# Kernel tuning notes

Measured on AMD Instinct MI355X. Metric: run time of the kernel, lower is better.

## Reference

```python
import jax, jax.numpy as jnp
import numpy as np

DIM = 96
NUM_HEADS = 6
KSIZE = 3
DILATIONS = (1, 2, 3)
HEAD_DIM = DIM // NUM_HEADS            # 16
NUM_DIL = len(DILATIONS)
GROUP_DIM = DIM // NUM_DIL             # 32 channels per dilation branch
MLP_HIDDEN = int(DIM * 4.0)
SCALE = HEAD_DIM ** -0.5
EPS = 1e-5


def _unfold(x, k, dil):
    """nn.Unfold(k, dilation=dil, padding=dil*(k-1)//2, stride=1).
    x: (B, C, H, W) -> (B, C, k*k, H, W), kernel positions row-major."""
    B, C, H, W = x.shape
    pad = dil * (k - 1) // 2
    xp = jnp.pad(x, ((0, 0), (0, 0), (pad, pad), (pad, pad)))
    pats = [xp[:, :, i * dil:i * dil + H, j * dil:j * dil + W]
            for i in range(k) for j in range(k)]
    return jnp.stack(pats, axis=2)  # (B, C, kk, H, W)


def _layernorm(x, w, b):
    mu = jnp.mean(x, axis=-1, keepdims=True)
    var = jnp.mean(jnp.square(x - mu), axis=-1, keepdims=True)
    return (x - mu) * jax.lax.rsqrt(var + EPS) * w + b


def _dilate_attention(q, k, v, dil):
    """q,k,v: (B, GROUP_DIM, H, W) -> (B, H, W, GROUP_DIM)."""
    B, gd, H, W = q.shape
    h = gd // HEAD_DIM
    kk = KSIZE * KSIZE
    HW = H * W
    qf = q.reshape(B, h, HEAD_DIM, HW)                      # bhdn
    ku = _unfold(k, KSIZE, dil).reshape(B, h, HEAD_DIM, kk, HW)  # bhdkn
    attn = jnp.einsum('bhdn,bhdkn->bhnk', qf, ku) * SCALE   # (B,h,HW,kk)
    attn = jax.nn.softmax(attn, axis=-1)
    vu = _unfold(v, KSIZE, dil).reshape(B, h, HEAD_DIM, kk, HW)
    out = jnp.einsum('bhnk,bhdkn->bnhd', attn, vu)          # (B,HW,h,HEAD_DIM)
    return out.reshape(B, H, W, gd)


def setup_inputs() -> dict:
    key = jax.random.key(0)
    ks = jax.random.split(key, 8)
    B, H, W = 8, 128, 128
    s = 0.02
    return {
        'x': jax.random.normal(ks[0], (B, DIM, H, W), jnp.float32),
        'qkv_w': jax.random.normal(ks[1], (3 * DIM, DIM), jnp.float32) * s,
        'proj_w': jax.random.normal(ks[2], (DIM, DIM), jnp.float32) * s,
        'proj_b': jnp.zeros((DIM,), jnp.float32),
        'ln1_w': jnp.ones((DIM,), jnp.float32),
        'ln1_b': jnp.zeros((DIM,), jnp.float32),
        'ln2_w': jnp.ones((DIM,), jnp.float32),
        'ln2_b': jnp.zeros((DIM,), jnp.float32),
        'fc1_w': jax.random.normal(ks[3], (MLP_HIDDEN, DIM), jnp.float32) * s,
        'fc1_b': jnp.zeros((MLP_HIDDEN,), jnp.float32),
        'fc2_w': jax.random.normal(ks[4], (DIM, MLP_HIDDEN), jnp.float32) * s,
        'fc2_b': jnp.zeros((DIM,), jnp.float32),
    }


def reference(x, qkv_w, proj_w, proj_b, ln1_w, ln1_b, ln2_w, ln2_b,
              fc1_w, fc1_b, fc2_w, fc2_b):
    B, C, H, W = x.shape
    xhw = jnp.transpose(x, (0, 2, 3, 1))                    # (B,H,W,C)

    # --- attention branch ---
    y = _layernorm(xhw, ln1_w, ln1_b)                       # (B,H,W,C)
    # qkv 1x1 conv == per-pixel matmul; output channel layout (3, nd, gd)
    qkv = jnp.einsum('bhwc,oc->bohw', y, qkv_w)             # (B,3C,H,W)
    qkv = qkv.reshape(B, 3, NUM_DIL, GROUP_DIM, H, W)
    outs = [
        _dilate_attention(qkv[:, 0, i], qkv[:, 1, i], qkv[:, 2, i], DILATIONS[i])
        for i in range(NUM_DIL)
    ]
    attn_out = jnp.concatenate(outs, axis=-1)               # (B,H,W,C)
    attn_out = jnp.einsum('bhwc,oc->bhwo', attn_out, proj_w) + proj_b
    xhw = xhw + attn_out

    # --- MLP branch ---
    y = _layernorm(xhw, ln2_w, ln2_b)
    h1 = jax.nn.gelu(jnp.einsum('bhwc,oc->bhwo', y, fc1_w) + fc1_b,
                     approximate=False)
    mlp_out = jnp.einsum('bhwc,oc->bhwo', h1, fc2_w) + fc2_b
    xhw = xhw + mlp_out

    return jnp.transpose(xhw, (0, 3, 1, 2))                 # (B,C,H,W)
```

## Files before the change

kernel.cpp:

```cpp
#include <hip/hip_runtime.h>
#include <hip/hip_bf16.h>
#include <math.h>

typedef __attribute__((ext_vector_type(8))) short bf16x8;
typedef __attribute__((ext_vector_type(4))) float f32x4;
typedef __attribute__((ext_vector_type(2))) unsigned u32x2;

#define MTOT  131072
#define HW16K 16384

__device__ inline float bf2f(unsigned short u) {
    union { unsigned u; float f; } x; x.u = ((unsigned)u) << 16; return x.f;
}
__device__ inline unsigned short f2bf(float a) {
    __hip_bfloat16 h = __float2bfloat16(a);
    union { __hip_bfloat16 h; unsigned short u; } c; c.h = h; return c.u;
}
__device__ inline unsigned pack2bf(float a, float b) {
    __hip_bfloat162 h = __float22bfloat162_rn(make_float2(a, b));
    union { __hip_bfloat162 h; unsigned u; } c; c.h = h; return c.u;
}
__device__ inline float gelu(float v) {
    float u = v * fmaf(0.07135481f, v * v, 1.5957691f);
    return __fdividef(v, 1.f + __expf(-u));
}
__device__ inline void load16(const unsigned short* p, float* f) {
    uint4 u0 = *(const uint4*)p;
    uint4 u1 = *(const uint4*)(p + 8);
    unsigned w[8] = {u0.x, u0.y, u0.z, u0.w, u1.x, u1.y, u1.z, u1.w};
#pragma unroll
    for (int i = 0; i < 8; i++) {
        union { unsigned u; float f; } lo, hi;
        lo.u = w[i] << 16; hi.u = w[i] & 0xffff0000u;
        f[2 * i] = lo.f; f[2 * i + 1] = hi.f;
    }
}

__global__ __launch_bounds__(256) void k_prep(const float* __restrict__ qw,
                                              const float* __restrict__ pw,
                                              const float* __restrict__ f1,
                                              const float* __restrict__ f2,
                                              const float* __restrict__ pb,
                                              const float* __restrict__ l2w,
                                              const float* __restrict__ l2b,
                                              const float* __restrict__ f2b,
                                              unsigned short* __restrict__ wq,
                                              unsigned short* __restrict__ wpt,
                                              unsigned short* __restrict__ w1t,
                                              unsigned short* __restrict__ w2t,
                                              float* __restrict__ scal) {
    int t = blockIdx.x * 256 + threadIdx.x;
    if (t < 27648) {
        int row = t / 96, col = t - row * 96;
        int s = row / 96;
        int rem = row - s * 96;
        int di = rem >> 5;
        int hd = (rem >> 4) & 1;
        int c  = rem & 15;
        int nrow = s * 96 + (di * 2 + hd) * 16 + c;
        wq[nrow * 96 + col] = f2bf(qw[t]);
    }
    else if (t < 36864) {
        int t2 = t - 27648;
        int och = t2 / 96, ich = t2 - och * 96;
        int nt = ((och >> 5) << 1) + ((och >> 2) & 1);
        int j  = ((och >> 3) & 3) * 4 + (och & 3);
        wpt[((nt * 3 + (ich >> 5)) * 16 + j) * 32 + (ich & 31)] = f2bf(pw[t2]);
    }
    else if (t < 73728) {
        int t2 = t - 36864;
        int och = t2 / 96, col = t2 - och * 96;
        int f  = och >> 5;
        int p  = och & 31;
        int q  = p >> 3, tt = (p >> 2) & 1, r = p & 3;
        int tile = f * 2 + tt;
        int j = q * 4 + r;
        w1t[((tile * 3 + (col >> 5)) * 16 + j) * 32 + (col & 31)] = f2bf(f1[t2]);
    }
    else if (t < 110592) {
        int t3 = t - 73728;
        int och = t3 / 384, ich = t3 - och * 384;
        int nt = ((och >> 5) << 1) + ((och >> 2) & 1);
        int j  = ((och >> 3) & 3) * 4 + (och & 3);
        w2t[((nt * 12 + (ich >> 5)) * 16 + j) * 32 + (ich & 31)] = f2bf(f2[t3]);
    }
    else if (t < 110976) {
        int i = t - 110592;
        int s = i / 96, slot = i - s * 96;
        int nt = slot >> 4, qq = (slot >> 2) & 3, r = slot & 3;
        int c = ((nt >> 1) << 5) + qq * 8 + ((nt & 1) << 2) + r;
        const float* src = (s == 0) ? pb : (s == 1) ? l2w : (s == 2) ? l2b : f2b;
        scal[i] = src[c];
    }
}

__global__ __launch_bounds__(512) void k_ln1qkv(const float* __restrict__ x,
                                                const float* __restrict__ w,
                                                const float* __restrict__ bln,
                                                const unsigned short* __restrict__ wq,
                                                unsigned short* __restrict__ qkvb) {
    __shared__ unsigned short bufbf[256 * 100];
    __shared__ unsigned short Bs[288 * 104];
    __shared__ float ps[512], ps2[512];
    int tid = threadIdx.x;
    int gp0 = blockIdx.x * 256;
    int b = gp0 >> 14, pix0 = gp0 & 16383;
    int p = tid & 255, half = tid >> 8;

    for (int i = tid; i < 3456; i += 512) {
        int row = i / 12, col = i - row * 12;
        *(uint4*)(Bs + row * 104 + col * 8) = ((const uint4*)wq)[i];
    }

    float val[48];
    float s = 0.f, s2 = 0.f;
#pragma unroll
    for (int i = 0; i < 48; i++) {
        int c = half * 48 + i;
        float v = x[((size_t)b * 96 + c) * HW16K + pix0 + p];
        val[i] = v; s += v; s2 += v * v;
    }
    ps[tid] = s; ps2[tid] = s2;
    __syncthreads();
    float st = ps[p] + ps[p + 256];
    float st2 = ps2[p] + ps2[p + 256];
    float mu = st * (1.f / 96.f);
    float inv = rsqrtf(st2 * (1.f / 96.f) - mu * mu + 1e-5f);
#pragma unroll
    for (int i = 0; i < 24; i++) {
        int c = half * 48 + 2 * i;
        float n0 = (val[2 * i] - mu) * inv * w[c] + bln[c];
        float n1 = (val[2 * i + 1] - mu) * inv * w[c + 1] + bln[c + 1];
        *(unsigned*)(bufbf + p * 100 + c) = pack2bf(n0, n1);
    }
    __syncthreads();

    int lane = tid & 63, wv = tid >> 6;
    int q = lane >> 4, l15 = lane & 15;
#pragma unroll 1
    for (int it = 0; it < 2; it++) {
        int pxl = (wv * 2 + it) * 16 + l15;
        bf16x8 pf[3];
#pragma unroll
        for (int f = 0; f < 3; f++)
            pf[f] = *(const bf16x8*)(bufbf + pxl * 100 + q * 8 + f * 32);
        int gpx = gp0 + pxl;
#pragma unroll
        for (int nt = 0; nt < 18; nt++) {
            f32x4 acc = (f32x4){0.f, 0.f, 0.f, 0.f};
#pragma unroll
            for (int f = 0; f < 3; f++) {
                bf16x8 wf = *(const bf16x8*)(Bs + (nt * 16 + l15) * 104 + q * 8 + f * 32);
                acc = __builtin_amdgcn_mfma_f32_16x16x32_bf16(wf, pf[f], acc, 0, 0, 0);
            }
            u32x2 pk = { pack2bf(acc[0], acc[1]), pack2bf(acc[2], acc[3]) };
            __builtin_nontemporal_store(pk,
                (u32x2*)(qkvb + ((size_t)nt * MTOT + gpx) * 16 + q * 4));
        }
    }
}

__global__ __launch_bounds__(256) void k_attn(const unsigned short* __restrict__ qkvb,
                                              unsigned short* __restrict__ attnb) {
    int bid = blockIdx.x;
    int xcd = bid & 7;
    int idx = bid >> 3;
    int g   = idx >> 6;
    int yb  = (xcd << 6) | (idx & 63);
    int px  = yb * 256 + threadIdx.x;

    int d = (g >> 1) + 1;
    int pix = px & 16383;
    int hh = pix >> 7, ww = pix & 127;
    int ibase = px & ~16383;

    const unsigned short* qpl = qkvb + (size_t)g * (MTOT * 16);
    const unsigned short* kpl = qkvb + (size_t)(6 + g) * (MTOT * 16);
    const unsigned short* vpl = qkvb + (size_t)(12 + g) * (MTOT * 16);

    float q[16];
    load16(qpl + (size_t)px * 16, q);

    float sc[9]; int nloc[9]; bool ok[9];
#pragma unroll
    for (int i = 0; i < 3; i++) {
#pragma unroll
        for (int j = 0; j < 3; j++) {
            int k9 = i * 3 + j;
            int yy = hh + (i - 1) * d;
            int xx = ww + (j - 1) * d;
            bool o_ = ((unsigned)yy < 128u) && ((unsigned)xx < 128u);
            ok[k9] = o_;
            nloc[k9] = ibase + yy * 128 + xx;
            float s = 0.f;
            if (o_) {
                float kf[16];
                load16(kpl + (size_t)nloc[k9] * 16, kf);
#pragma unroll
                for (int c = 0; c < 16; c++) s += q[c] * kf[c];
            }
            sc[k9] = s * 0.25f;
        }
    }
    float mx = sc[0];
#pragma unroll
    for (int k9 = 1; k9 < 9; k9++) mx = fmaxf(mx, sc[k9]);
    float sum = 0.f;
#pragma unroll
    for (int k9 = 0; k9 < 9; k9++) { sc[k9] = __expf(sc[k9] - mx); sum += sc[k9]; }
    float rs = 1.f / sum;

    float o[16];
#pragma unroll
    for (int c = 0; c < 16; c++) o[c] = 0.f;
#pragma unroll
    for (int k9 = 0; k9 < 9; k9++) {
        if (ok[k9]) {
            float vf[16];
            load16(vpl + (size_t)nloc[k9] * 16, vf);
            float w9 = sc[k9];
#pragma unroll
            for (int c = 0; c < 16; c++) o[c] += w9 * vf[c];
        }
    }
    uint4* orow = (uint4*)(attnb + ((size_t)g * MTOT + px) * 16);
    uint4 pk0;
    pk0.x = pack2bf(o[0] * rs, o[1] * rs);
    pk0.y = pack2bf(o[2] * rs, o[3] * rs);
    pk0.z = pack2bf(o[4] * rs, o[5] * rs);
    pk0.w = pack2bf(o[6] * rs, o[7] * rs);
    orow[0] = pk0;
    uint4 pk1;
    pk1.x = pack2bf(o[8] * rs, o[9] * rs);
    pk1.y = pack2bf(o[10] * rs, o[11] * rs);
    pk1.z = pack2bf(o[12] * rs, o[13] * rs);
    pk1.w = pack2bf(o[14] * rs, o[15] * rs);
    orow[1] = pk1;
}

__global__ __launch_bounds__(256) void k_pmlp(const unsigned short* __restrict__ attnb,
                                              const unsigned short* __restrict__ wpt,
                                              const float* __restrict__ scal,
                                              const float* __restrict__ x,
                                              const unsigned short* __restrict__ w1t,
                                              const float* __restrict__ b1,
                                              const unsigned short* __restrict__ w2t,
                                              float* __restrict__ out) {
    int tid = threadIdx.x;
    int lane = tid & 63, wv = tid >> 6;
    int q = lane >> 4, l15 = lane & 15;
    int pt0 = (blockIdx.x * 4 + wv) * 2;
    int px0 = pt0 * 16 + l15;
    int px1 = px0 + 16;

    float v0[24], v1[24];
    bf16x8 a0[3], a1[3];

#define PROJ_TILE(PX, V, A)                                                      \
    do {                                                                         \
        bf16x8 pf[3];                                                            \
        _Pragma("unroll")                                                        \
        for (int f = 0; f < 3; f++) {                                            \
            int pa = 2 * f + (q >> 1);                                           \
            pf[f] = *(const bf16x8*)(attnb + ((size_t)pa * MTOT + (PX)) * 16 + (q & 1) * 8); \
        }                                                                        \
        f32x4 acc[6];                                                            \
        _Pragma("unroll")                                                        \
        for (int nt = 0; nt < 6; nt++) acc[nt] = (f32x4){0.f, 0.f, 0.f, 0.f};    \
        _Pragma("unroll")                                                        \
        for (int nt = 0; nt < 6; nt++) {                                         \
            _Pragma("unroll")                                                    \
            for (int kf = 0; kf < 3; kf++) {                                     \
                bf16x8 wf = *(const bf16x8*)(wpt + ((nt * 3 + kf) * 16 + l15) * 32 + q * 8); \
                acc[nt] = __builtin_amdgcn_mfma_f32_16x16x32_bf16(wf, pf[kf], acc[nt], 0, 0, 0); \
            }                                                                    \
        }                                                                        \
        int bb_ = (PX) >> 14, pix_ = (PX) & 16383;                               \
        float s_ = 0.f, s2_ = 0.f;                                               \
        _Pragma("unroll")                                                        \
        for (int nt = 0; nt < 6; nt++) {                                         \
            float4 pbq = ((const float4*)scal)[nt * 4 + q];                      \
            int cb = ((nt >> 1) << 5) + q * 8 + ((nt & 1) << 2);                 \
            _Pragma("unroll")                                                    \
            for (int r = 0; r < 4; r++) {                                        \
                float xv = x[((size_t)bb_ * 96 + cb + r) * HW16K + pix_];        \
                float t_ = acc[nt][r] + ((&pbq.x)[r]) + xv;                      \
                V[nt * 4 + r] = t_; s_ += t_; s2_ += t_ * t_;                    \
            }                                                                    \
        }                                                                        \
        s_ += __shfl_xor(s_, 16);  s_ += __shfl_xor(s_, 32);                     \
        s2_ += __shfl_xor(s2_, 16); s2_ += __shfl_xor(s2_, 32);                  \
        float mu_ = s_ * (1.f / 96.f);                                           \
        float inv_ = rsqrtf(s2_ * (1.f / 96.f) - mu_ * mu_ + 1e-5f);             \
        float nrm[24];                                                           \
        _Pragma("unroll")                                                        \
        for (int nt = 0; nt < 6; nt++) {                                         \
            float4 lwq = ((const float4*)(scal + 96))[nt * 4 + q];               \
            float4 lbq = ((const float4*)(scal + 192))[nt * 4 + q];              \
            _Pragma("unroll")                                                    \
            for (int r = 0; r < 4; r++)                                          \
                nrm[nt * 4 + r] = (V[nt * 4 + r] - mu_) * inv_ * ((&lwq.x)[r]) + ((&lbq.x)[r]); \
        }                                                                        \
        _Pragma("unroll")                                                        \
        for (int kf = 0; kf < 3; kf++) {                                         \
            union { unsigned u[4]; bf16x8 v; } Hh;                               \
            Hh.u[0] = pack2bf(nrm[(kf * 2) * 4 + 0], nrm[(kf * 2) * 4 + 1]);     \
            Hh.u[1] = pack2bf(nrm[(kf * 2) * 4 + 2], nrm[(kf * 2) * 4 + 3]);     \
            Hh.u[2] = pack2bf(nrm[(kf * 2 + 1) * 4 + 0], nrm[(kf * 2 + 1) * 4 + 1]); \
            Hh.u[3] = pack2bf(nrm[(kf * 2 + 1) * 4 + 2], nrm[(kf * 2 + 1) * 4 + 3]); \
            A[kf] = Hh.v;                                                        \
        }                                                                        \
    } while (0)

    PROJ_TILE(px0, v0, a0);
    PROJ_TILE(px1, v1, a1);
#undef PROJ_TILE

    f32x4 acc2a[6], acc2b[6];
#pragma unroll
    for (int nt = 0; nt < 6; nt++) {
        acc2a[nt] = (f32x4){0.f, 0.f, 0.f, 0.f};
        acc2b[nt] = (f32x4){0.f, 0.f, 0.f, 0.f};
    }

#pragma unroll 1
    for (int f = 0; f < 12; f++) {
        bf16x8 wf0[3], wf1[3];
#pragma unroll
        for (int kf = 0; kf < 3; kf++) {
            wf0[kf] = *(const bf16x8*)(w1t + (((2 * f) * 3 + kf) * 16 + l15) * 32 + q * 8);
            wf1[kf] = *(const bf16x8*)(w1t + (((2 * f + 1) * 3 + kf) * 16 + l15) * 32 + q * 8);
        }
        f32x4 c00 = (f32x4){0.f,0.f,0.f,0.f}, c01 = (f32x4){0.f,0.f,0.f,0.f};
        f32x4 c10 = (f32x4){0.f,0.f,0.f,0.f}, c11 = (f32x4){0.f,0.f,0.f,0.f};
#pragma unroll
        for (int kf = 0; kf < 3; kf++) {
            c00 = __builtin_amdgcn_mfma_f32_16x16x32_bf16(wf0[kf], a0[kf], c00, 0, 0, 0);
            c01 = __builtin_amdgcn_mfma_f32_16x16x32_bf16(wf1[kf], a0[kf], c01, 0, 0, 0);
            c10 = __builtin_amdgcn_mfma_f32_16x16x32_bf16(wf0[kf], a1[kf], c10, 0, 0, 0);
            c11 = __builtin_amdgcn_mfma_f32_16x16x32_bf16(wf1[kf], a1[kf], c11, 0, 0, 0);
        }
        bf16x8 w2f[6];
#pragma unroll
        for (int nt = 0; nt < 6; nt++)
            w2f[nt] = *(const bf16x8*)(w2t + ((nt * 12 + f) * 16 + l15) * 32 + q * 8);

        float4 bb0 = ((const float4*)b1)[8 * f + 2 * q];
        float4 bb1 = ((const float4*)b1)[8 * f + 2 * q + 1];
        union { unsigned u[4]; bf16x8 v; } H0, H1;
        H0.u[0] = pack2bf(gelu(c00[0] + bb0.x), gelu(c00[1] + bb0.y));
        H0.u[1] = pack2bf(gelu(c00[2] + bb0.z), gelu(c00[3] + bb0.w));
        H0.u[2] = pack2bf(gelu(c01[0] + bb1.x), gelu(c01[1] + bb1.y));
        H0.u[3] = pack2bf(gelu(c01[2] + bb1.z), gelu(c01[3] + bb1.w));
        H1.u[0] = pack2bf(gelu(c10[0] + bb0.x), gelu(c10[1] + bb0.y));
        H1.u[1] = pack2bf(gelu(c10[2] + bb0.z), gelu(c10[3] + bb0.w));
        H1.u[2] = pack2bf(gelu(c11[0] + bb1.x), gelu(c11[1] + bb1.y));
        H1.u[3] = pack2bf(gelu(c11[2] + bb1.z), gelu(c11[3] + bb1.w));

#pragma unroll
        for (int nt = 0; nt < 6; nt++) {
            acc2a[nt] = __builtin_amdgcn_mfma_f32_16x16x32_bf16(w2f[nt], H0.v, acc2a[nt], 0, 0, 0);
            acc2b[nt] = __builtin_amdgcn_mfma_f32_16x16x32_bf16(w2f[nt], H1.v, acc2b[nt], 0, 0, 0);
        }
    }

    int b0 = px0 >> 14, pia = px0 & 16383;
    int b1i = px1 >> 14, pib = px1 & 16383;
#pragma unroll
    for (int nt = 0; nt < 6; nt++) {
        float4 b2q = ((const float4*)(scal + 288))[nt * 4 + q];
        int cb = ((nt >> 1) << 5) + q * 8 + ((nt & 1) << 2);
#pragma unroll
        for (int r = 0; r < 4; r++) {
            float ov0 = acc2a[nt][r] + ((&b2q.x)[r]) + v0[nt * 4 + r];
            __builtin_nontemporal_store(ov0, out + ((size_t)b0 * 96 + cb + r) * HW16K + pia);
            float ov1 = acc2b[nt][r] + ((&b2q.x)[r]) + v1[nt * 4 + r];
            __builtin_nontemporal_store(ov1, out + ((size_t)b1i * 96 + cb + r) * HW16K + pib);
        }
    }
}

extern "C" void kernel_launch(void* const* d_in, const int* in_sizes, int n_in,
                              void* d_out, int out_size, void* d_ws, size_t ws_size,
                              hipStream_t stream) {
    const float* x      = (const float*)d_in[0];
    const float* qkv_w  = (const float*)d_in[1];
    const float* proj_w = (const float*)d_in[2];
    const float* proj_b = (const float*)d_in[3];
    const float* ln1w   = (const float*)d_in[4];
    const float* ln1b   = (const float*)d_in[5];
    const float* ln2w   = (const float*)d_in[6];
    const float* ln2b   = (const float*)d_in[7];
    const float* fc1w   = (const float*)d_in[8];
    const float* fc1b   = (const float*)d_in[9];
    const float* fc2w   = (const float*)d_in[10];
    const float* fc2b   = (const float*)d_in[11];
    float* out = (float*)d_out;

    char* ws = (char*)d_ws;
    unsigned short* wq   = (unsigned short*)(ws);
    unsigned short* wpt  = (unsigned short*)(ws + 55296);
    unsigned short* w1t  = (unsigned short*)(ws + 73728);
    unsigned short* w2t  = (unsigned short*)(ws + 147456);
    float*          scal = (float*)(ws + 221184);
    unsigned short* rA   = (unsigned short*)(ws + 230400);
    unsigned short* qkvb = (unsigned short*)(ws + 25396224);

    k_prep<<<434, 256, 0, stream>>>(qkv_w, proj_w, fc1w, fc2w,
                                    proj_b, ln2w, ln2b, fc2b,
                                    wq, wpt, w1t, w2t, scal);

    k_ln1qkv<<<512, 512, 0, stream>>>(x, ln1w, ln1b, wq, qkvb);
    k_attn<<<3072, 256, 0, stream>>>(qkvb, rA);
    k_pmlp<<<1024, 256, 0, stream>>>(rA, wpt, scal, x, w1t, fc1b, w2t, out);
}
```

Baseline: 238.8 us.

## Pre-tile QKV weights, enlarge LN1-QKV blocks, and use shuffle-based LayerNorm reduction

QKV weights are now written by the prep kernel in MFMA-tile order, so they can be copied to LDS contiguously without padding. The LN1+QKV kernel now uses 1024-thread blocks covering 512 pixels, with each wave owning 32 pixels split into two channel halves. The mean/variance reduction uses a cross-lane shuffle instead of shared memory plus a barrier. This lowers how many times the weights are staged per pixel and removes a sync, but the LDS footprint grows to about 154KB, limiting occupancy to one block per CU.

Measured after the change: 286.5 us. +20.0%, slower.

```diff
diff --git a/kernel.cpp b/kernel.cpp
--- a/kernel.cpp
+++ b/kernel.cpp
@@ -44,7 +44,7 @@
                                               const float* __restrict__ l2w,
                                               const float* __restrict__ l2b,
                                               const float* __restrict__ f2b,
-                                              unsigned short* __restrict__ wq,
+                                              unsigned short* __restrict__ wqt,
                                               unsigned short* __restrict__ wpt,
                                               unsigned short* __restrict__ w1t,
                                               unsigned short* __restrict__ w2t,
@@ -58,7 +58,8 @@
         int hd = (rem >> 4) & 1;
         int c  = rem & 15;
         int nrow = s * 96 + (di * 2 + hd) * 16 + c;
-        wq[nrow * 96 + col] = f2bf(qw[t]);
+        wqt[(((nrow >> 4) * 3 + (col >> 5)) * 16 + (nrow & 15)) * 32 + (col & 31)]
+            = f2bf(qw[t]);
     }
     else if (t < 36864) {
         int t2 = t - 27648;
@@ -94,23 +95,22 @@
     }
 }
 
-__global__ __launch_bounds__(512) void k_ln1qkv(const float* __restrict__ x,
-                                                const float* __restrict__ w,
-                                                const float* __restrict__ bln,
-                                                const unsigned short* __restrict__ wq,
-                                                unsigned short* __restrict__ qkvb) {
-    __shared__ unsigned short bufbf[256 * 100];
-    __shared__ unsigned short Bs[288 * 104];
-    __shared__ float ps[512], ps2[512];
+__global__ __launch_bounds__(1024) void k_ln1qkv(const float* __restrict__ x,
+                                                 const float* __restrict__ w,
+                                                 const float* __restrict__ bln,
+                                                 const unsigned short* __restrict__ wqt,
+                                                 unsigned short* __restrict__ qkvb) {
+    __shared__ unsigned short bufbf[512 * 100];
+    __shared__ unsigned short Bs[288 * 96];
     int tid = threadIdx.x;
-    int gp0 = blockIdx.x * 256;
+    int gp0 = blockIdx.x * 512;
     int b = gp0 >> 14, pix0 = gp0 & 16383;
-    int p = tid & 255, half = tid >> 8;
-
-    for (int i = tid; i < 3456; i += 512) {
-        int row = i / 12, col = i - row * 12;
-        *(uint4*)(Bs + row * 104 + col * 8) = ((const uint4*)wq)[i];
-    }
+    int lane = tid & 63, wv = tid >> 6;
+    int half = lane >> 5;
+    int p = wv * 32 + (lane & 31);
+
+    for (int i = tid; i < 3456; i += 1024)
+        ((uint4*)Bs)[i] = ((const uint4*)wqt)[i];
 
     float val[48];
     float s = 0.f, s2 = 0.f;
@@ -120,12 +120,10 @@
         float v = x[((size_t)b * 96 + c) * HW16K + pix0 + p];
         val[i] = v; s += v; s2 += v * v;
     }
-    ps[tid] = s; ps2[tid] = s2;
-    __syncthreads();
-    float st = ps[p] + ps[p + 256];
-    float st2 = ps2[p] + ps2[p + 256];
-    float mu = st * (1.f / 96.f);
-    float inv = rsqrtf(st2 * (1.f / 96.f) - mu * mu + 1e-5f);
+    s += __shfl_xor(s, 32);
+    s2 += __shfl_xor(s2, 32);
+    float mu = s * (1.f / 96.f);
+    float inv = rsqrtf(s2 * (1.f / 96.f) - mu * mu + 1e-5f);
 #pragma unroll
     for (int i = 0; i < 24; i++) {
         int c = half * 48 + 2 * i;
@@ -135,7 +133,6 @@
     }
     __syncthreads();
 
-    int lane = tid & 63, wv = tid >> 6;
     int q = lane >> 4, l15 = lane & 15;
 #pragma unroll 1
     for (int it = 0; it < 2; it++) {
@@ -149,9 +146,9 @@
         for (int nt = 0; nt < 18; nt++) {
             f32x4 acc = (f32x4){0.f, 0.f, 0.f, 0.f};
 #pragma unroll
-            for (int f = 0; f < 3; f++) {
-                bf16x8 wf = *(const bf16x8*)(Bs + (nt * 16 + l15) * 104 + q * 8 + f * 32);
-                acc = __builtin_amdgcn_mfma_f32_16x16x32_bf16(wf, pf[f], acc, 0, 0, 0);
+            for (int kf = 0; kf < 3; kf++) {
+                bf16x8 wf = *(const bf16x8*)(Bs + ((nt * 3 + kf) * 16 + l15) * 32 + q * 8);
+                acc = __builtin_amdgcn_mfma_f32_16x16x32_bf16(wf, pf[kf], acc, 0, 0, 0);
             }
             u32x2 pk = { pack2bf(acc[0], acc[1]), pack2bf(acc[2], acc[3]) };
             __builtin_nontemporal_store(pk,
@@ -398,7 +395,7 @@
     float* out = (float*)d_out;
 
     char* ws = (char*)d_ws;
-    unsigned short* wq   = (unsigned short*)(ws);
+    unsigned short* wqt  = (unsigned short*)(ws);
     unsigned short* wpt  = (unsigned short*)(ws + 55296);
     unsigned short* w1t  = (unsigned short*)(ws + 73728);
     unsigned short* w2t  = (unsigned short*)(ws + 147456);
@@ -408,9 +405,9 @@
 
     k_prep<<<434, 256, 0, stream>>>(qkv_w, proj_w, fc1w, fc2w,
                                     proj_b, ln2w, ln2b, fc2b,
-                                    wq, wpt, w1t, w2t, scal);
-
-    k_ln1qkv<<<512, 512, 0, stream>>>(x, ln1w, ln1b, wq, qkvb);
+                                    wqt, wpt, w1t, w2t, scal);
+
+    k_ln1qkv<<<256, 1024, 0, stream>>>(x, ln1w, ln1b, wqt, qkvb);
     k_attn<<<3072, 256, 0, stream>>>(qkvb, rA);
     k_pmlp<<<1024, 256, 0, stream>>>(rA, wpt, scal, x, w1t, fc1b, w2t, out);
 }
```
